# Performance work log

Hardware: AMD Instinct MI355X
Metric: run time of the kernel (lower is better)

## Reference

```python
import jax, jax.numpy as jnp
import numpy as np

D = 192          # embed_dim
DI = 2 * D       # d_inner (Mamba expand=2)
R = 12           # dt_rank = ceil(D / d_state)
N = 16           # d_state
DEPTH = 24
P = 16           # patch size
B = 4
SS, TS = 256, 128
PT = (TS // P) ** 2   # 64 template patches
PS = (SS // P) ** 2   # 256 search patches
L = PT + PS + 1       # 321 tokens (middle cls)


def setup_inputs() -> dict:
    key = jax.random.key(0)
    ks = jax.random.split(key, 24)
    f = lambda k, shp, s=0.02: (jax.random.normal(k, shp) * s).astype(jnp.float32)
    Alog = jnp.log(jnp.arange(1, N + 1, dtype=jnp.float32))  # S4D-real init
    Alog = jnp.tile(Alog, (DEPTH, DI, 1))
    return {
        "x_search": f(ks[0], (B, 3, SS, SS), 1.0),
        "x_template": f(ks[1], (B, 3, TS, TS), 1.0),
        "patch_w": f(ks[2], (D, 3, P, P)),
        "patch_b": jnp.zeros((D,), jnp.float32),
        "cls_token": f(ks[3], (1, 1, D)),
        "pos_embed": f(ks[4], (1, L, D)),
        "Win": f(ks[5], (DEPTH, 2 * DI, D)),
        "convw": f(ks[6], (DEPTH, DI, 4), 0.2),
        "convb": jnp.zeros((DEPTH, DI), jnp.float32),
        "Wx": f(ks[7], (DEPTH, R + 2 * N, DI)),
        "Wdt": f(ks[8], (DEPTH, DI, R), 0.1),
        "bdt": f(ks[9], (DEPTH, DI), 0.1),
        "Alog": Alog,
        "Dp": jnp.ones((DEPTH, DI), jnp.float32),
        "convw_b": f(ks[10], (DEPTH, DI, 4), 0.2),
        "convb_b": jnp.zeros((DEPTH, DI), jnp.float32),
        "Wx_b": f(ks[11], (DEPTH, R + 2 * N, DI)),
        "Wdt_b": f(ks[12], (DEPTH, DI, R), 0.1),
        "bdt_b": f(ks[13], (DEPTH, DI), 0.1),
        "Alog_b": Alog,
        "Dp_b": jnp.ones((DEPTH, DI), jnp.float32),
        "Wout": f(ks[14], (DEPTH, D, DI)),
        "normw": jnp.ones((DEPTH, D), jnp.float32),
        "normw_f": jnp.ones((D,), jnp.float32),
    }


def silu(x):
    return x * jax.nn.sigmoid(x)


def rmsnorm(x, w, eps=1e-5):
    return x * jax.lax.rsqrt(jnp.mean(x * x, -1, keepdims=True) + eps) * w


def patch_embed(x, w, b):
    # non-overlapping patch conv == blocked reshape + einsum
    Bn, C, H, W = x.shape
    xp = x.reshape(Bn, C, H // P, P, W // P, P)
    t = jnp.einsum('bcipjq,dcpq->bijd', xp, w)
    return t.reshape(Bn, (H // P) * (W // P), -1) + b


def causal_conv(u, w, b):
    # depthwise causal conv, kernel 4: u [B,DI,L], w [DI,4]
    Lx = u.shape[-1]
    up = jnp.pad(u, ((0, 0), (0, 0), (3, 0)))
    y = sum(w[:, k][None, :, None] * up[:, :, k:k + Lx] for k in range(4))
    return y + b[None, :, None]


def selective_scan(u, delta, A, Bm, Cm, Dp):
    # u, delta: [B,DI,L]; A: [DI,N]; Bm, Cm: [B,N,L]
    dA = jnp.exp(jnp.einsum('bdl,dn->lbdn', delta, A))
    dBu = jnp.einsum('bdl,bnl->lbdn', delta * u, Bm)

    def step(h, inp):
        dAt, dBut, ct = inp
        h = dAt * h + dBut
        return h, jnp.einsum('bdn,bn->bd', h, ct)

    h0 = jnp.zeros((u.shape[0], DI, N), u.dtype)
    _, ys = jax.lax.scan(step, h0, (dA, dBu, Cm.transpose(2, 0, 1)))
    y = ys.transpose(1, 2, 0)  # [B,DI,L]
    return y + Dp[None, :, None] * u


def _branch(x, z, convw, convb, Wx, Wdt, bdt, Alog, Dp):
    xc = silu(causal_conv(x, convw, convb))
    xdbl = jnp.einsum('bdl,ed->ble', xc, Wx)
    dt, Bm, Cm = xdbl[..., :R], xdbl[..., R:R + N], xdbl[..., R + N:]
    delta = jax.nn.softplus(jnp.einsum('blr,dr->bdl', dt, Wdt) + bdt[None, :, None])
    y = selective_scan(xc, delta, -jnp.exp(Alog), Bm.transpose(0, 2, 1),
                       Cm.transpose(0, 2, 1), Dp)
    return y * silu(z)


def _mixer(h, p):
    xz = jnp.einsum('bld,ed->ble', h, p['Win'])
    x = xz[..., :DI].transpose(0, 2, 1)   # [B,DI,L]
    z = xz[..., DI:].transpose(0, 2, 1)
    y = _branch(x, z, p['convw'], p['convb'], p['Wx'], p['Wdt'], p['bdt'],
                p['Alog'], p['Dp'])
    yb = _branch(x[..., ::-1], z[..., ::-1], p['convw_b'], p['convb_b'], p['Wx_b'],
                 p['Wdt_b'], p['bdt_b'], p['Alog_b'], p['Dp_b'])
    out = (y + yb[..., ::-1]) * 0.5  # bimamba v2 with if_divide_out
    return jnp.einsum('bdl,od->blo', out, p['Wout'])


def reference(x_search, x_template, patch_w, patch_b, cls_token, pos_embed,
              Win, convw, convb, Wx, Wdt, bdt, Alog, Dp,
              convw_b, convb_b, Wx_b, Wdt_b, bdt_b, Alog_b, Dp_b,
              Wout, normw, normw_f):
    ts = patch_embed(x_template, patch_w, patch_b)   # [B,64,D]
    ss = patch_embed(x_search, patch_w, patch_b)     # [B,256,D]
    tok = jnp.concatenate([ts, ss], 1)               # [B,320,D]
    mid = tok.shape[1] // 2
    cls = jnp.broadcast_to(cls_token, (tok.shape[0], 1, D))
    tok = jnp.concatenate([tok[:, :mid], cls, tok[:, mid:]], 1) + pos_embed

    lp = {'Win': Win, 'convw': convw, 'convb': convb, 'Wx': Wx, 'Wdt': Wdt,
          'bdt': bdt, 'Alog': Alog, 'Dp': Dp, 'convw_b': convw_b,
          'convb_b': convb_b, 'Wx_b': Wx_b, 'Wdt_b': Wdt_b, 'bdt_b': bdt_b,
          'Alog_b': Alog_b, 'Dp_b': Dp_b, 'Wout': Wout, 'normw': normw}

    def layer_step(carry, p):
        hidden, residual = carry
        residual = hidden + residual           # add
        hn = rmsnorm(residual, p['normw'])     # norm (fused_add_norm semantics)
        hidden = _mixer(hn, p)                 # mamba mixer
        return (hidden, residual), None

    (hidden, residual), _ = jax.lax.scan(layer_step, (tok, jnp.zeros_like(tok)), lp)
    return rmsnorm(hidden + residual, normw_f)   # final add + norm, [B,321,D]
```

## Files before the change

kernel.cpp:

```cpp
#include <hip/hip_runtime.h>
#include <math.h>

#define B_ 4
#define L_ 321
#define D_ 192
#define DI_ 384
#define E_ 768
#define R_ 12
#define N_ 16
#define DEPTH_ 24
#define XD 44

#define NC_ 21
#define LC_ 16

typedef __attribute__((ext_vector_type(8))) short bf16x8;
typedef __attribute__((ext_vector_type(4))) float f32x4;
typedef unsigned short ushort_t;

__device__ __forceinline__ float silu_f(float x) { return x / (1.f + __expf(-x)); }

__device__ __forceinline__ ushort_t f2bf(float x) {
    union { float f; unsigned u; } v; v.f = x;
    return (ushort_t)((v.u + 0x7fffu + ((v.u >> 16) & 1u)) >> 16);
}
__device__ __forceinline__ float bf2f(ushort_t h) {
    union { unsigned u; float f; } v; v.u = ((unsigned)h) << 16; return v.f;
}

__global__ void cvt_bf16(const float* __restrict__ src, ushort_t* __restrict__ dst, int n) {
    for (int i = blockIdx.x * blockDim.x + threadIdx.x; i < n; i += gridDim.x * blockDim.x)
        dst[i] = f2bf(src[i]);
}

__global__ void im2col_kernel(const float* __restrict__ xs, const float* __restrict__ xt,
                              ushort_t* __restrict__ pm) {
    int p_all = blockIdx.x % 320;
    int b = blockIdx.x / 320;
    const float* src; int i, j, W;
    if (p_all < 64) { int p = p_all; i = p >> 3; j = p & 7; W = 128; src = xt + (size_t)b*3*128*128; }
    else            { int p = p_all - 64; i = p >> 4; j = p & 15; W = 256; src = xs + (size_t)b*3*256*256; }
    ushort_t* dst = pm + (size_t)blockIdx.x * 768;
    for (int m = threadIdx.x; m < 768; m += blockDim.x) {
        int c = m >> 8, rem = m & 255, pp = rem >> 4, qq = rem & 15;
        dst[m] = f2bf(src[(size_t)(c*W + i*16 + pp)*W + j*16 + qq]);
    }
}

__global__ void tok_scatter(const float* __restrict__ tokmat, const float* __restrict__ pb,
                            const float* __restrict__ cls, const float* __restrict__ pos,
                            float* __restrict__ hidden, float* __restrict__ residual) {
    int blk = blockIdx.x;
    int b = blk / L_, t = blk % L_;
    int d = threadIdx.x;
    size_t o = (size_t)(b*L_ + t)*D_ + d;
    residual[o] = 0.f;
    float v;
    if (t == 160) v = cls[d];
    else {
        int p = (t < 160) ? t : t - 1;
        v = tokmat[(size_t)(b*320 + p)*D_ + d] + pb[d];
    }
    hidden[o] = v + pos[t*D_ + d];
}

template<int WM, int WN, int MFR, int NFR, int CMODE>
__global__ __launch_bounds__(WM*WN*64) void mfma_gemm(const ushort_t* __restrict__ A,
                          const ushort_t* __restrict__ Bw,
                          float* __restrict__ Cf, ushort_t* __restrict__ Ch,
                          int M, int N, int K) {
    constexpr int BM = WM * MFR * 16;
    constexpr int BN = WN * NFR * 16;
    int bx = blockIdx.x, by = blockIdx.y;
    int wave = threadIdx.x >> 6, lane = threadIdx.x & 63;
    int wr = wave / WN, wc = wave % WN;
    int m0 = by * BM + wr * MFR * 16;
    int n0 = bx * BN + wc * NFR * 16;
    int lrow = lane & 15;
    int lk   = (lane >> 4) * 8;

    f32x4 acc[MFR][NFR];
#pragma unroll
    for (int i = 0; i < MFR; ++i)
#pragma unroll
        for (int j = 0; j < NFR; ++j) acc[i][j] = (f32x4){0.f, 0.f, 0.f, 0.f};

    for (int k0 = 0; k0 < K; k0 += 32) {
        bf16x8 a[MFR], b[NFR];
#pragma unroll
        for (int i = 0; i < MFR; ++i) {
            int r = m0 + i*16 + lrow; r = min(r, M - 1);
            a[i] = *(const bf16x8*)(A + (size_t)r*K + k0 + lk);
        }
#pragma unroll
        for (int jn = 0; jn < NFR; ++jn) {
            int c = n0 + jn*16 + lrow; c = min(c, N - 1);
            b[jn] = *(const bf16x8*)(Bw + (size_t)c*K + k0 + lk);
        }
#pragma unroll
        for (int i = 0; i < MFR; ++i)
#pragma unroll
            for (int jn = 0; jn < NFR; ++jn)
                acc[i][jn] = __builtin_amdgcn_mfma_f32_16x16x32_bf16(a[i], b[jn], acc[i][jn], 0, 0, 0);
    }

    int crow = (lane >> 4) * 4;
    int ccol = lane & 15;
#pragma unroll
    for (int i = 0; i < MFR; ++i)
#pragma unroll
        for (int jn = 0; jn < NFR; ++jn) {
            int c = n0 + jn*16 + ccol;
            if (c >= N) continue;
#pragma unroll
            for (int j = 0; j < 4; ++j) {
                int r = m0 + i*16 + crow + j;
                if (r < M) {
                    if (CMODE == 0) Cf[(size_t)r*N + c] = acc[i][jn][j];
                    else            Ch[(size_t)r*N + c] = f2bf(acc[i][jn][j]);
                }
            }
        }
}

__global__ __launch_bounds__(64) void xdbl_dual(
    const ushort_t* __restrict__ xcf, const ushort_t* __restrict__ xcb,
    const ushort_t* __restrict__ Wxf, const ushort_t* __restrict__ Wxbw,
    float* __restrict__ xdf, float* __restrict__ xdb) {
    const int M = B_ * L_;
    int rev = blockIdx.y;
    const ushort_t* A  = rev ? xcb : xcf;
    const ushort_t* Bw = rev ? Wxbw : Wxf;
    float* C = rev ? xdb : xdf;
    int lane = threadIdx.x;
    int m0 = blockIdx.x * 16;
    int lrow = lane & 15, lk = (lane >> 4) * 8;

    f32x4 acc[3];
#pragma unroll
    for (int jn = 0; jn < 3; ++jn) acc[jn] = (f32x4){0.f, 0.f, 0.f, 0.f};

    for (int k0 = 0; k0 < DI_; k0 += 32) {
        int r = min(m0 + lrow, M - 1);
        bf16x8 a = *(const bf16x8*)(A + (size_t)r*DI_ + k0 + lk);
        bf16x8 b[3];
#pragma unroll
        for (int jn = 0; jn < 3; ++jn) {
            int c = min(jn*16 + lrow, XD - 1);
            b[jn] = *(const bf16x8*)(Bw + (size_t)c*DI_ + k0 + lk);
        }
#pragma unroll
        for (int jn = 0; jn < 3; ++jn)
            acc[jn] = __builtin_amdgcn_mfma_f32_16x16x32_bf16(a, b[jn], acc[jn], 0, 0, 0);
    }
    int crow = (lane >> 4) * 4, ccol = lane & 15;
#pragma unroll
    for (int jn = 0; jn < 3; ++jn) {
        int c = jn*16 + ccol;
        if (c >= XD) continue;
#pragma unroll
        for (int j = 0; j < 4; ++j) {
            int r = m0 + crow + j;
            if (r < M) C[(size_t)r*XD + c] = acc[jn][j];
        }
    }
}

__global__ __launch_bounds__(64) void outproj_gemm(
    const float* __restrict__ yf, const float* __restrict__ yb,
    const ushort_t* __restrict__ Ww, float* __restrict__ hidden) {
    const int M = B_*L_, Nn = D_, K = DI_;
    int lane = threadIdx.x;
    int m0 = blockIdx.y * 32;
    int n0 = blockIdx.x * 48;
    int lrow = lane & 15, lk = (lane >> 4) * 8;

    f32x4 acc[2][3];
#pragma unroll
    for (int i = 0; i < 2; ++i)
#pragma unroll
        for (int jn = 0; jn < 3; ++jn) acc[i][jn] = (f32x4){0.f, 0.f, 0.f, 0.f};

    for (int k0 = 0; k0 < K; k0 += 32) {
        bf16x8 a[2];
#pragma unroll
        for (int i = 0; i < 2; ++i) {
            int r = min(m0 + i*16 + lrow, M - 1);
            const float* p0 = yf + (size_t)r*K + k0 + lk;
            const float* p1 = yb + (size_t)r*K + k0 + lk;
            bf16x8 t;
#pragma unroll
            for (int j = 0; j < 8; ++j) t[j] = (short)f2bf(0.5f*(p0[j] + p1[j]));
            a[i] = t;
        }
        bf16x8 b[3];
#pragma unroll
        for (int jn = 0; jn < 3; ++jn) {
            int c = n0 + jn*16 + lrow;
            b[jn] = *(const bf16x8*)(Ww + (size_t)c*K + k0 + lk);
        }
#pragma unroll
        for (int i = 0; i < 2; ++i)
#pragma unroll
            for (int jn = 0; jn < 3; ++jn)
                acc[i][jn] = __builtin_amdgcn_mfma_f32_16x16x32_bf16(a[i], b[jn], acc[i][jn], 0, 0, 0);
    }
    int crow = (lane >> 4) * 4, ccol = lane & 15;
#pragma unroll
    for (int i = 0; i < 2; ++i)
#pragma unroll
        for (int jn = 0; jn < 3; ++jn) {
            int c = n0 + jn*16 + ccol;
#pragma unroll
            for (int j = 0; j < 4; ++j) {
                int r = m0 + i*16 + crow + j;
                if (r < M) hidden[(size_t)r*Nn + c] = acc[i][jn][j];
            }
        }
}

__global__ void prenorm_kernel(float* __restrict__ residual, const float* __restrict__ hidden,
                               const float* __restrict__ normw, ushort_t* __restrict__ hn) {
    int row = blockIdx.x;
    int tid = threadIdx.x;
    __shared__ float red[256];
    float v = 0.f;
    if (tid < D_) {
        v = residual[(size_t)row*D_ + tid] + hidden[(size_t)row*D_ + tid];
        residual[(size_t)row*D_ + tid] = v;
    }
    red[tid] = v * v;
    __syncthreads();
    for (int s = 128; s > 0; s >>= 1) { if (tid < s) red[tid] += red[tid + s]; __syncthreads(); }
    float scale = rsqrtf(red[0] / (float)D_ + 1e-5f);
    if (tid < D_) hn[(size_t)row*D_ + tid] = f2bf(v * scale * normw[tid]);
}

__global__ void final_kernel(const float* __restrict__ residual, const float* __restrict__ hidden,
                             const float* __restrict__ normw_f, float* __restrict__ out) {
    int row = blockIdx.x;
    int tid = threadIdx.x;
    __shared__ float red[256];
    float v = 0.f;
    if (tid < D_) v = residual[(size_t)row*D_ + tid] + hidden[(size_t)row*D_ + tid];
    red[tid] = v * v;
    __syncthreads();
    for (int s = 128; s > 0; s >>= 1) { if (tid < s) red[tid] += red[tid + s]; __syncthreads(); }
    float scale = rsqrtf(red[0] / (float)D_ + 1e-5f);
    if (tid < D_) out[(size_t)row*D_ + tid] = v * scale * normw_f[tid];
}

__global__ void conv_kernel(const ushort_t* __restrict__ xz,
                            const float* __restrict__ cw, const float* __restrict__ cb,
                            const float* __restrict__ cwb, const float* __restrict__ cbb,
                            ushort_t* __restrict__ xc_f, ushort_t* __restrict__ xc_b) {
    int blk = blockIdx.x;
    int b = blk / L_, l = blk % L_;
    int d = threadIdx.x;
    const ushort_t* xbase = xz + (size_t)b*L_*E_ + d;
    float acc = cb[d];
#pragma unroll
    for (int k = 0; k < 4; ++k) {
        int t = l - 3 + k;
        if (t >= 0) acc = fmaf(cw[d*4 + k], bf2f(xbase[(size_t)t*E_]), acc);
    }
    xc_f[(size_t)(b*L_ + l)*DI_ + d] = f2bf(silu_f(acc));
    float accb = cbb[d];
#pragma unroll
    for (int k = 0; k < 4; ++k) {
        int t = l - 3 + k;
        if (t >= 0) accb = fmaf(cwb[d*4 + k], bf2f(xbase[(size_t)(L_ - 1 - t)*E_]), accb);
    }
    xc_b[(size_t)(b*L_ + l)*DI_ + d] = f2bf(silu_f(accb));
}

__global__ __launch_bounds__(192) void scan_part1(
                           const ushort_t* __restrict__ xc_f, const ushort_t* __restrict__ xc_b,
                           const float* __restrict__ xdbl_f, const float* __restrict__ xdbl_b,
                           const float* __restrict__ Wdt, const float* __restrict__ bdt,
                           const float* __restrict__ Wdtb, const float* __restrict__ bdtb,
                           const float* __restrict__ Alog, const float* __restrict__ Alogb,
                           float* __restrict__ hloc, float* __restrict__ aprod) {
    int c = blockIdx.x, b = blockIdx.y >> 1, half = blockIdx.y & 1, br = blockIdx.z;
    int tid = threadIdx.x;
    int d = half * 192 + tid;
    const ushort_t* xc = br ? xc_b : xc_f;
    const float* xd = br ? xdbl_b : xdbl_f;
    const float* Wd = br ? Wdtb : Wdt;
    const float* bd = br ? bdtb : bdt;
    const float* Al = br ? Alogb : Alog;
    __shared__ float su[LC_][192];
    __shared__ float sdt[LC_][R_];
    __shared__ float sB[LC_][N_];
    int lbeg = c * LC_;
    int lend = min(lbeg + LC_, L_);
    int len = lend - lbeg;
    for (int l2 = 0; l2 < len; ++l2) {
        size_t row = (size_t)b*L_ + lbeg + l2;
        su[l2][tid] = bf2f(xc[row*DI_ + d]);
    }
    for (int idx = tid; idx < len*N_; idx += 192) {
        int l2 = idx >> 4, n = idx & 15;
        sB[l2][n] = xd[((size_t)b*L_ + lbeg + l2)*XD + R_ + n];
    }
    for (int idx = tid; idx < len*R_; idx += 192) {
        int l2 = idx / R_, r = idx % R_;
        sdt[l2][r] = xd[((size_t)b*L_ + lbeg + l2)*XD + r];
    }
    __syncthreads();
    float wreg[R_];
#pragma unroll
    for (int r = 0; r < R_; ++r) wreg[r] = Wd[d*R_ + r];
    float bdv = bd[d];
    float a[N_];
#pragma unroll
    for (int n = 0; n < N_; ++n) a[n] = -__expf(Al[d*N_ + n]);
    float h[N_], ap[N_];
#pragma unroll
    for (int n = 0; n < N_; ++n) { h[n] = 0.f; ap[n] = 1.f; }

    auto step = [&](int l2) {
        float dacc = bdv;
#pragma unroll
        for (int r = 0; r < R_; ++r) dacc = fmaf(wreg[r], sdt[l2][r], dacc);
        float dv = fmaxf(dacc, 0.f) + log1pf(__expf(-fabsf(dacc)));
        float u = su[l2][tid], du = dv * u;
#pragma unroll
        for (int n = 0; n < N_; ++n) {
            float e = __expf(dv * a[n]);
            h[n] = fmaf(e, h[n], du * sB[l2][n]);
            ap[n] *= e;
        }
    };
    if (len == LC_) {
#pragma unroll 4
        for (int l2 = 0; l2 < LC_; ++l2) step(l2);
    } else {
        for (int l2 = 0; l2 < len; ++l2) step(l2);
    }
    size_t base = (((size_t)(b*2 + br)*NC_ + c)*N_)*DI_ + d;
#pragma unroll
    for (int n = 0; n < N_; ++n) {
        hloc[base + (size_t)n*DI_]  = h[n];
        aprod[base + (size_t)n*DI_] = ap[n];
    }
}

__global__ void scan_combine(const float* __restrict__ hloc, const float* __restrict__ aprod,
                             float* __restrict__ hin) {
    int g = blockIdx.x * blockDim.x + threadIdx.x;
    int bb = g / (N_ * DI_);
    int rem = g % (N_ * DI_);
    float hrun = 0.f;
    for (int c = 0; c < NC_; ++c) {
        size_t idx = ((size_t)bb*NC_ + c)*N_*DI_ + rem;
        hin[idx] = hrun;
        hrun = fmaf(aprod[idx], hrun, hloc[idx]);
    }
}

__global__ __launch_bounds__(192) void scan_part3(
                           const ushort_t* __restrict__ xc_f, const ushort_t* __restrict__ xc_b,
                           const float* __restrict__ xdbl_f, const float* __restrict__ xdbl_b,
                           const float* __restrict__ Wdt, const float* __restrict__ bdt,
                           const float* __restrict__ Wdtb, const float* __restrict__ bdtb,
                           const ushort_t* __restrict__ xz,
                           const float* __restrict__ Alog, const float* __restrict__ Alogb,
                           const float* __restrict__ Dpf, const float* __restrict__ Dpb,
                           const float* __restrict__ hin,
                           float* __restrict__ y_f, float* __restrict__ y_b) {
    int c = blockIdx.x, b = blockIdx.y >> 1, half = blockIdx.y & 1, br = blockIdx.z;
    int tid = threadIdx.x;
    int d = half * 192 + tid;
    const ushort_t* xc = br ? xc_b : xc_f;
    const float* xd = br ? xdbl_b : xdbl_f;
    const float* Wd = br ? Wdtb : Wdt;
    const float* bd = br ? bdtb : bdt;
    const float* Al = br ? Alogb : Alog;
    const float* Dpp = br ? Dpb : Dpf;
    float* y = br ? y_b : y_f;
    __shared__ float su[LC_][192];
    __shared__ float sdt[LC_][R_];
    __shared__ float sB[LC_][N_];
    __shared__ float sC[LC_][N_];
    int lbeg = c * LC_;
    int lend = min(lbeg + LC_, L_);
    int len = lend - lbeg;
    for (int l2 = 0; l2 < len; ++l2) {
        size_t row = (size_t)b*L_ + lbeg + l2;
        su[l2][tid] = bf2f(xc[row*DI_ + d]);
    }
    for (int idx = tid; idx < len*N_; idx += 192) {
        int l2 = idx >> 4, n = idx & 15;
        size_t row = (size_t)b*L_ + lbeg + l2;
        sB[l2][n] = xd[row*XD + R_ + n];
        sC[l2][n] = xd[row*XD + R_ + N_ + n];
    }
    for (int idx = tid; idx < len*R_; idx += 192) {
        int l2 = idx / R_, r = idx % R_;
        sdt[l2][r] = xd[((size_t)b*L_ + lbeg + l2)*XD + r];
    }
    __syncthreads();
    float wreg[R_];
#pragma unroll
    for (int r = 0; r < R_; ++r) wreg[r] = Wd[d*R_ + r];
    float bdv = bd[d];
    float a[N_];
#pragma unroll
    for (int n = 0; n < N_; ++n) a[n] = -__expf(Al[d*N_ + n]);
    float h[N_];
    size_t hbase = (((size_t)(b*2 + br)*NC_ + c)*N_)*DI_ + d;
#pragma unroll
    for (int n = 0; n < N_; ++n) h[n] = hin[hbase + (size_t)n*DI_];
    float dpv = Dpp[d];

    auto step = [&](int l2) {
        float dacc = bdv;
#pragma unroll
        for (int r = 0; r < R_; ++r) dacc = fmaf(wreg[r], sdt[l2][r], dacc);
        float dv = fmaxf(dacc, 0.f) + log1pf(__expf(-fabsf(dacc)));
        float u = su[l2][tid], du = dv * u;
        float yv = 0.f;
#pragma unroll
        for (int n = 0; n < N_; ++n) {
            float e = __expf(dv * a[n]);
            h[n] = fmaf(e, h[n], du * sB[l2][n]);
            yv = fmaf(h[n], sC[l2][n], yv);
        }
        yv = fmaf(dpv, u, yv);
        int lo = br ? (L_ - 1 - (lbeg + l2)) : (lbeg + l2);
        float zv = bf2f(xz[((size_t)b*L_ + lo)*E_ + DI_ + d]);
        y[((size_t)b*L_ + lo)*DI_ + d] = yv * silu_f(zv);
    };
    if (len == LC_) {
#pragma unroll 4
        for (int l2 = 0; l2 < LC_; ++l2) step(l2);
    } else {
        for (int l2 = 0; l2 < len; ++l2) step(l2);
    }
}

extern "C" void kernel_launch(void* const* d_in, const int* in_sizes, int n_in,
                              void* d_out, int out_size, void* d_ws, size_t ws_size,
                              hipStream_t stream) {
    const float* xs     = (const float*)d_in[0];
    const float* xt     = (const float*)d_in[1];
    const float* pw     = (const float*)d_in[2];
    const float* pb     = (const float*)d_in[3];
    const float* cls    = (const float*)d_in[4];
    const float* pos    = (const float*)d_in[5];
    const float* Win    = (const float*)d_in[6];
    const float* convw  = (const float*)d_in[7];
    const float* convb  = (const float*)d_in[8];
    const float* Wx     = (const float*)d_in[9];
    const float* Wdt    = (const float*)d_in[10];
    const float* bdt    = (const float*)d_in[11];
    const float* Alog   = (const float*)d_in[12];
    const float* Dp     = (const float*)d_in[13];
    const float* convwb = (const float*)d_in[14];
    const float* convbb = (const float*)d_in[15];
    const float* Wxb    = (const float*)d_in[16];
    const float* Wdtb   = (const float*)d_in[17];
    const float* bdtb   = (const float*)d_in[18];
    const float* Alogb  = (const float*)d_in[19];
    const float* Dpb    = (const float*)d_in[20];
    const float* Wout   = (const float*)d_in[21];
    const float* normw  = (const float*)d_in[22];
    const float* normwf = (const float*)d_in[23];
    float* out = (float*)d_out;

    float* ws = (float*)d_ws;
    size_t off = 0;
    auto alloc = [&](size_t nfloats) { float* p = ws + off; off += nfloats; return p; };
    const size_t BL = (size_t)B_ * L_;
    const size_t CHNK = (size_t)B_ * 2 * NC_ * N_ * DI_;

    float*    residual = alloc(BL * D_);
    float*    hidden   = alloc(BL * D_);
    ushort_t* hn_bf    = (ushort_t*)alloc(BL * D_ / 2);
    ushort_t* xzb_bf   = (ushort_t*)alloc(BL * E_ / 2);
    ushort_t* xcf_bf   = (ushort_t*)alloc(BL * DI_ / 2);
    ushort_t* xcb_bf   = (ushort_t*)alloc(BL * DI_ / 2);
    float*    xdbl_f   = alloc(BL * XD);
    float*    xdbl_b   = alloc(BL * XD);
    float*    y_f      = alloc(BL * DI_);
    float*    y_b      = alloc(BL * DI_);
    float*    hloc     = alloc(CHNK);
    float*    aprod    = alloc(CHNK);
    float*    hin      = alloc(CHNK);
    ushort_t* pw_bf    = (ushort_t*)alloc((size_t)D_ * 768 / 2);
    ushort_t* Win_bf   = (ushort_t*)alloc((size_t)DEPTH_ * E_ * D_ / 2);
    ushort_t* Wx_bf    = (ushort_t*)alloc((size_t)DEPTH_ * XD * DI_ / 2);
    ushort_t* Wxb_bf   = (ushort_t*)alloc((size_t)DEPTH_ * XD * DI_ / 2);
    ushort_t* Wout_bf  = (ushort_t*)alloc((size_t)DEPTH_ * D_ * DI_ / 2);
    (void)ws_size; (void)in_sizes; (void)n_in; (void)out_size;

    cvt_bf16<<<dim3(64),   dim3(256), 0, stream>>>(pw,   pw_bf,   D_ * 768);
    cvt_bf16<<<dim3(2048), dim3(256), 0, stream>>>(Win,  Win_bf,  DEPTH_ * E_ * D_);
    cvt_bf16<<<dim3(512),  dim3(256), 0, stream>>>(Wx,   Wx_bf,   DEPTH_ * XD * DI_);
    cvt_bf16<<<dim3(512),  dim3(256), 0, stream>>>(Wxb,  Wxb_bf,  DEPTH_ * XD * DI_);
    cvt_bf16<<<dim3(1024), dim3(256), 0, stream>>>(Wout, Wout_bf, DEPTH_ * D_ * DI_);

    ushort_t* pmat   = (ushort_t*)y_f;
    float*    tokmat = y_b;
    im2col_kernel<<<dim3(B_ * 320), dim3(256), 0, stream>>>(xs, xt, pmat);
    mfma_gemm<2, 2, 2, 2, 0><<<dim3(3, 20), dim3(256), 0, stream>>>(
        pmat, pw_bf, tokmat, nullptr, B_ * 320, D_, 768);
    tok_scatter<<<dim3(B_ * L_), dim3(192), 0, stream>>>(tokmat, pb, cls, pos, hidden, residual);

    for (int layer = 0; layer < DEPTH_; ++layer) {
        const ushort_t* Win_l  = Win_bf  + (size_t)layer * E_ * D_;
        const ushort_t* Wx_l   = Wx_bf   + (size_t)layer * XD * DI_;
        const ushort_t* Wxb_l  = Wxb_bf  + (size_t)layer * XD * DI_;
        const ushort_t* Wout_l = Wout_bf + (size_t)layer * D_ * DI_;
        const float* cw_l    = convw  + (size_t)layer * DI_ * 4;
        const float* cb_l    = convb  + (size_t)layer * DI_;
        const float* cwb_l   = convwb + (size_t)layer * DI_ * 4;
        const float* cbb_l   = convbb + (size_t)layer * DI_;
        const float* Wdt_l   = Wdt    + (size_t)layer * DI_ * R_;
        const float* Wdtb_l  = Wdtb   + (size_t)layer * DI_ * R_;
        const float* bdt_l   = bdt    + (size_t)layer * DI_;
        const float* bdtb_l  = bdtb   + (size_t)layer * DI_;
        const float* Alog_l  = Alog   + (size_t)layer * DI_ * N_;
        const float* Alogb_l = Alogb  + (size_t)layer * DI_ * N_;
        const float* Dp_l    = Dp     + (size_t)layer * DI_;
        const float* Dpb_l   = Dpb    + (size_t)layer * DI_;
        const float* normw_l = normw  + (size_t)layer * D_;

        prenorm_kernel<<<dim3((int)BL), dim3(256), 0, stream>>>(residual, hidden, normw_l, hn_bf);
        mfma_gemm<2, 2, 2, 2, 1><<<dim3(12, 21), dim3(256), 0, stream>>>(
            hn_bf, Win_l, nullptr, xzb_bf, (int)BL, E_, D_);
        conv_kernel<<<dim3((int)BL), dim3(DI_), 0, stream>>>(
            xzb_bf, cw_l, cb_l, cwb_l, cbb_l, xcf_bf, xcb_bf);
        xdbl_dual<<<dim3(81, 2), dim3(64), 0, stream>>>(
            xcf_bf, xcb_bf, Wx_l, Wxb_l, xdbl_f, xdbl_b);
        scan_part1<<<dim3(NC_, B_ * 2, 2), dim3(192), 0, stream>>>(
            xcf_bf, xcb_bf, xdbl_f, xdbl_b, Wdt_l, bdt_l, Wdtb_l, bdtb_l,
            Alog_l, Alogb_l, hloc, aprod);
        scan_combine<<<dim3((B_*2*N_*DI_)/256), dim3(256), 0, stream>>>(hloc, aprod, hin);
        scan_part3<<<dim3(NC_, B_ * 2, 2), dim3(192), 0, stream>>>(
            xcf_bf, xcb_bf, xdbl_f, xdbl_b, Wdt_l, bdt_l, Wdtb_l, bdtb_l, xzb_bf,
            Alog_l, Alogb_l, Dp_l, Dpb_l, hin, y_f, y_b);
        outproj_gemm<<<dim3(4, 41), dim3(64), 0, stream>>>(y_f, y_b, Wout_l, hidden);
    }

    final_kernel<<<dim3((int)BL), dim3(256), 0, stream>>>(residual, hidden, normwf, out);
}
```

Measured before the change: 1.941 ms.

## Fuse in-projection with causal conv and out-projection with residual-add RMSNorm

Merges the in-projection GEMM with the depthwise causal conv (forward and reversed), so the x-half stays in shared memory and only z is written. The out-projection now adds the residual and applies the next layer's RMSNorm in its epilogue, which removes the separate prenorm and final kernels and the hidden buffer. The scan kernels read u straight into registers instead of staging it in shared memory. This cuts launches and global round-trips, at the cost of recomputing three halo rows per tile and running the out-projection as a 16-row grid with a cross-wave reduction.

```diff
diff --git a/kernel.cpp b/kernel.cpp
--- a/kernel.cpp
+++ b/kernel.cpp
@@ -49,25 +49,35 @@
 
 __global__ void tok_scatter(const float* __restrict__ tokmat, const float* __restrict__ pb,
                             const float* __restrict__ cls, const float* __restrict__ pos,
-                            float* __restrict__ hidden, float* __restrict__ residual) {
+                            float* __restrict__ residual) {
     int blk = blockIdx.x;
     int b = blk / L_, t = blk % L_;
     int d = threadIdx.x;
-    size_t o = (size_t)(b*L_ + t)*D_ + d;
-    residual[o] = 0.f;
     float v;
     if (t == 160) v = cls[d];
     else {
         int p = (t < 160) ? t : t - 1;
         v = tokmat[(size_t)(b*320 + p)*D_ + d] + pb[d];
     }
-    hidden[o] = v + pos[t*D_ + d];
-}
-
-template<int WM, int WN, int MFR, int NFR, int CMODE>
+    residual[(size_t)(b*L_ + t)*D_ + d] = v + pos[t*D_ + d];
+}
+
+__global__ void rms0_kernel(const float* __restrict__ residual, const float* __restrict__ normw,
+                            ushort_t* __restrict__ hn) {
+    int row = blockIdx.x;
+    int tid = threadIdx.x;
+    __shared__ float red[256];
+    float v = (tid < D_) ? residual[(size_t)row*D_ + tid] : 0.f;
+    red[tid] = v * v;
+    __syncthreads();
+    for (int s = 128; s > 0; s >>= 1) { if (tid < s) red[tid] += red[tid + s]; __syncthreads(); }
+    float scale = rsqrtf(red[0] / (float)D_ + 1e-5f);
+    if (tid < D_) hn[(size_t)row*D_ + tid] = f2bf(v * scale * normw[tid]);
+}
+
+template<int WM, int WN, int MFR, int NFR>
 __global__ __launch_bounds__(WM*WN*64) void mfma_gemm(const ushort_t* __restrict__ A,
-                          const ushort_t* __restrict__ Bw,
-                          float* __restrict__ Cf, ushort_t* __restrict__ Ch,
+                          const ushort_t* __restrict__ Bw, float* __restrict__ Cf,
                           int M, int N, int K) {
     constexpr int BM = WM * MFR * 16;
     constexpr int BN = WN * NFR * 16;
@@ -115,12 +125,86 @@
 #pragma unroll
             for (int j = 0; j < 4; ++j) {
                 int r = m0 + i*16 + crow + j;
-                if (r < M) {
-                    if (CMODE == 0) Cf[(size_t)r*N + c] = acc[i][jn][j];
-                    else            Ch[(size_t)r*N + c] = f2bf(acc[i][jn][j]);
-                }
+                if (r < M) Cf[(size_t)r*N + c] = acc[i][jn][j];
             }
         }
+}
+
+__global__ __launch_bounds__(256) void inproj_conv(
+    const ushort_t* __restrict__ hn, const ushort_t* __restrict__ Win_l,
+    const float* __restrict__ cw, const float* __restrict__ cb,
+    const float* __restrict__ cwb, const float* __restrict__ cbb,
+    ushort_t* __restrict__ xc_f, ushort_t* __restrict__ xc_b,
+    ushort_t* __restrict__ zbuf) {
+    int bx = blockIdx.x, by = blockIdx.y;
+    int b = by / 6, lm0 = (by % 6) * 64;
+    int wave = threadIdx.x >> 6, lane = threadIdx.x & 63;
+    int lrow = lane & 15, lk = (lane >> 4) * 8;
+    int ecol0 = bx * 64 + wave * 16;
+    bool xp = bx < 6;
+    int nf = xp ? 5 : 4;
+    int lbase = xp ? lm0 - 3 : lm0;
+
+    __shared__ float xt[80][68];
+
+    f32x4 acc[5];
+#pragma unroll
+    for (int fi = 0; fi < 5; ++fi) acc[fi] = (f32x4){0.f, 0.f, 0.f, 0.f};
+
+    for (int k0 = 0; k0 < D_; k0 += 32) {
+        bf16x8 bw = *(const bf16x8*)(Win_l + (size_t)(ecol0 + lrow)*D_ + k0 + lk);
+        for (int fi = 0; fi < nf; ++fi) {
+            int l = lbase + fi*16 + lrow;
+            l = min(max(l, 0), L_ - 1);
+            bf16x8 af = *(const bf16x8*)(hn + (size_t)(b*L_ + l)*D_ + k0 + lk);
+            acc[fi] = __builtin_amdgcn_mfma_f32_16x16x32_bf16(af, bw, acc[fi], 0, 0, 0);
+        }
+    }
+
+    int crow = (lane >> 4) * 4, ccol = lane & 15;
+    if (!xp) {
+#pragma unroll
+        for (int fi = 0; fi < 4; ++fi)
+#pragma unroll
+            for (int j = 0; j < 4; ++j) {
+                int l = lm0 + fi*16 + crow + j;
+                if (l < L_) zbuf[(size_t)(b*L_ + l)*DI_ + (ecol0 + ccol - DI_)] = f2bf(acc[fi][j]);
+            }
+        return;
+    }
+#pragma unroll
+    for (int fi = 0; fi < 5; ++fi)
+#pragma unroll
+        for (int j = 0; j < 4; ++j)
+            xt[fi*16 + crow + j][wave*16 + ccol] = acc[fi][j];
+    __syncthreads();
+
+    int dc = threadIdx.x & 63;
+    int lofs = threadIdx.x >> 6;
+    int d = bx*64 + dc;
+    float4 wf = *(const float4*)(cw + (size_t)d*4);
+    float4 wb = *(const float4*)(cwb + (size_t)d*4);
+    float bf0 = cb[d], bb0 = cbb[d];
+#pragma unroll
+    for (int i = 0; i < 16; ++i) {
+        int l2 = lofs + i*4;
+        int lf = lm0 + l2;
+        if (lf < L_) {
+            float a0 = bf0;
+#pragma unroll
+            for (int k = 0; k < 4; ++k)
+                if (lf - 3 + k >= 0) a0 = fmaf(((const float*)&wf)[k], xt[l2 + k][dc], a0);
+            xc_f[(size_t)(b*L_ + lf)*DI_ + d] = f2bf(silu_f(a0));
+        }
+        int lpp = (L_ - 1) - lm0 - l2;
+        if (lpp >= 0) {
+            float a1 = bb0;
+#pragma unroll
+            for (int k = 0; k < 4; ++k)
+                if (lpp - 3 + k >= 0) a1 = fmaf(((const float*)&wb)[k], xt[l2 + 6 - k][dc], a1);
+            xc_b[(size_t)(b*L_ + lpp)*DI_ + d] = f2bf(silu_f(a1));
+        }
+    }
 }
 
 __global__ __launch_bounds__(64) void xdbl_dual(
@@ -166,33 +250,29 @@
     }
 }
 
-__global__ __launch_bounds__(64) void outproj_gemm(
+template<bool LAST>
+__global__ __launch_bounds__(256) void outproj_fused(
     const float* __restrict__ yf, const float* __restrict__ yb,
-    const ushort_t* __restrict__ Ww, float* __restrict__ hidden) {
+    const ushort_t* __restrict__ Ww,
+    float* __restrict__ residual, const float* __restrict__ nw,
+    ushort_t* __restrict__ hn, float* __restrict__ outp) {
     const int M = B_*L_, Nn = D_, K = DI_;
-    int lane = threadIdx.x;
-    int m0 = blockIdx.y * 32;
-    int n0 = blockIdx.x * 48;
+    int wave = threadIdx.x >> 6, lane = threadIdx.x & 63;
+    int m0 = blockIdx.x * 16;
+    int n0 = wave * 48;
     int lrow = lane & 15, lk = (lane >> 4) * 8;
 
-    f32x4 acc[2][3];
-#pragma unroll
-    for (int i = 0; i < 2; ++i)
-#pragma unroll
-        for (int jn = 0; jn < 3; ++jn) acc[i][jn] = (f32x4){0.f, 0.f, 0.f, 0.f};
+    f32x4 acc[3];
+#pragma unroll
+    for (int jn = 0; jn < 3; ++jn) acc[jn] = (f32x4){0.f, 0.f, 0.f, 0.f};
 
     for (int k0 = 0; k0 < K; k0 += 32) {
-        bf16x8 a[2];
-#pragma unroll
-        for (int i = 0; i < 2; ++i) {
-            int r = min(m0 + i*16 + lrow, M - 1);
-            const float* p0 = yf + (size_t)r*K + k0 + lk;
-            const float* p1 = yb + (size_t)r*K + k0 + lk;
-            bf16x8 t;
-#pragma unroll
-            for (int j = 0; j < 8; ++j) t[j] = (short)f2bf(0.5f*(p0[j] + p1[j]));
-            a[i] = t;
-        }
+        int r = min(m0 + lrow, M - 1);
+        const float* p0 = yf + (size_t)r*K + k0 + lk;
+        const float* p1 = yb + (size_t)r*K + k0 + lk;
+        bf16x8 a;
+#pragma unroll
+        for (int j = 0; j < 8; ++j) a[j] = (short)f2bf(0.5f*(p0[j] + p1[j]));
         bf16x8 b[3];
 #pragma unroll
         for (int jn = 0; jn < 3; ++jn) {
@@ -200,78 +280,55 @@
             b[jn] = *(const bf16x8*)(Ww + (size_t)c*K + k0 + lk);
         }
 #pragma unroll
-        for (int i = 0; i < 2; ++i)
-#pragma unroll
-            for (int jn = 0; jn < 3; ++jn)
-                acc[i][jn] = __builtin_amdgcn_mfma_f32_16x16x32_bf16(a[i], b[jn], acc[i][jn], 0, 0, 0);
-    }
+        for (int jn = 0; jn < 3; ++jn)
+            acc[jn] = __builtin_amdgcn_mfma_f32_16x16x32_bf16(a, b[jn], acc[jn], 0, 0, 0);
+    }
+
     int crow = (lane >> 4) * 4, ccol = lane & 15;
-#pragma unroll
-    for (int i = 0; i < 2; ++i)
+    float resv[4][3];
+    float sq[4] = {0.f, 0.f, 0.f, 0.f};
+#pragma unroll
+    for (int j = 0; j < 4; ++j) {
+        int r = m0 + crow + j;
+        bool ok = r < M;
 #pragma unroll
         for (int jn = 0; jn < 3; ++jn) {
             int c = n0 + jn*16 + ccol;
-#pragma unroll
-            for (int j = 0; j < 4; ++j) {
-                int r = m0 + i*16 + crow + j;
-                if (r < M) hidden[(size_t)r*Nn + c] = acc[i][jn][j];
+            float v = ok ? (residual[(size_t)r*Nn + c] + acc[jn][j]) : 0.f;
+            resv[j][jn] = v;
+            sq[j] = fmaf(v, v, sq[j]);
+        }
+    }
+#pragma unroll
+    for (int m = 1; m < 16; m <<= 1)
+#pragma unroll
+        for (int j = 0; j < 4; ++j) sq[j] += __shfl_xor(sq[j], m, 64);
+
+    __shared__ float part[16][4];
+    if (ccol == 0) {
+#pragma unroll
+        for (int j = 0; j < 4; ++j) part[crow + j][wave] = sq[j];
+    }
+    __syncthreads();
+#pragma unroll
+    for (int j = 0; j < 4; ++j) {
+        int r = m0 + crow + j;
+        if (r >= M) continue;
+        int rt = crow + j;
+        float tot = part[rt][0] + part[rt][1] + part[rt][2] + part[rt][3];
+        float scale = rsqrtf(tot / (float)Nn + 1e-5f);
+#pragma unroll
+        for (int jn = 0; jn < 3; ++jn) {
+            int c = n0 + jn*16 + ccol;
+            float v = resv[j][jn];
+            if (LAST) {
+                outp[(size_t)r*Nn + c] = v * scale * nw[c];
+            } else {
+                residual[(size_t)r*Nn + c] = v;
+                hn[(size_t)r*Nn + c] = f2bf(v * scale * nw[c]);
             }
         }
-}
-
-__global__ void prenorm_kernel(float* __restrict__ residual, const float* __restrict__ hidden,
-                               const float* __restrict__ normw, ushort_t* __restrict__ hn) {
-    int row = blockIdx.x;
-    int tid = threadIdx.x;
-    __shared__ float red[256];
-    float v = 0.f;
-    if (tid < D_) {
-        v = residual[(size_t)row*D_ + tid] + hidden[(size_t)row*D_ + tid];
-        residual[(size_t)row*D_ + tid] = v;
-    }
-    red[tid] = v * v;
-    __syncthreads();
-    for (int s = 128; s > 0; s >>= 1) { if (tid < s) red[tid] += red[tid + s]; __syncthreads(); }
-    float scale = rsqrtf(red[0] / (float)D_ + 1e-5f);
-    if (tid < D_) hn[(size_t)row*D_ + tid] = f2bf(v * scale * normw[tid]);
-}
-
-__global__ void final_kernel(const float* __restrict__ residual, const float* __restrict__ hidden,
-                             const float* __restrict__ normw_f, float* __restrict__ out) {
-    int row = blockIdx.x;
-    int tid = threadIdx.x;
-    __shared__ float red[256];
-    float v = 0.f;
-    if (tid < D_) v = residual[(size_t)row*D_ + tid] + hidden[(size_t)row*D_ + tid];
-    red[tid] = v * v;
-    __syncthreads();
-    for (int s = 128; s > 0; s >>= 1) { if (tid < s) red[tid] += red[tid + s]; __syncthreads(); }
-    float scale = rsqrtf(red[0] / (float)D_ + 1e-5f);
-    if (tid < D_) out[(size_t)row*D_ + tid] = v * scale * normw_f[tid];
-}
-
-__global__ void conv_kernel(const ushort_t* __restrict__ xz,
-                            const float* __restrict__ cw, const float* __restrict__ cb,
-                            const float* __restrict__ cwb, const float* __restrict__ cbb,
-                            ushort_t* __restrict__ xc_f, ushort_t* __restrict__ xc_b) {
-    int blk = blockIdx.x;
-    int b = blk / L_, l = blk % L_;
-    int d = threadIdx.x;
-    const ushort_t* xbase = xz + (size_t)b*L_*E_ + d;
-    float acc = cb[d];
-#pragma unroll
-    for (int k = 0; k < 4; ++k) {
-        int t = l - 3 + k;
-        if (t >= 0) acc = fmaf(cw[d*4 + k], bf2f(xbase[(size_t)t*E_]), acc);
-    }
-    xc_f[(size_t)(b*L_ + l)*DI_ + d] = f2bf(silu_f(acc));
-    float accb = cbb[d];
-#pragma unroll
-    for (int k = 0; k < 4; ++k) {
-        int t = l - 3 + k;
-        if (t >= 0) accb = fmaf(cwb[d*4 + k], bf2f(xbase[(size_t)(L_ - 1 - t)*E_]), accb);
-    }
-    xc_b[(size_t)(b*L_ + l)*DI_ + d] = f2bf(silu_f(accb));
+    }
 }
 
 __global__ __launch_bounds__(192) void scan_part1(
@@ -289,16 +346,10 @@
     const float* Wd = br ? Wdtb : Wdt;
     const float* bd = br ? bdtb : bdt;
     const float* Al = br ? Alogb : Alog;
-    __shared__ float su[LC_][192];
     __shared__ float sdt[LC_][R_];
     __shared__ float sB[LC_][N_];
     int lbeg = c * LC_;
-    int lend = min(lbeg + LC_, L_);
-    int len = lend - lbeg;
-    for (int l2 = 0; l2 < len; ++l2) {
-        size_t row = (size_t)b*L_ + lbeg + l2;
-        su[l2][tid] = bf2f(xc[row*DI_ + d]);
-    }
+    int len = min(lbeg + LC_, L_) - lbeg;
     for (int idx = tid; idx < len*N_; idx += 192) {
         int l2 = idx >> 4, n = idx & 15;
         sB[l2][n] = xd[((size_t)b*L_ + lbeg + l2)*XD + R_ + n];
@@ -319,12 +370,12 @@
 #pragma unroll
     for (int n = 0; n < N_; ++n) { h[n] = 0.f; ap[n] = 1.f; }
 
-    auto step = [&](int l2) {
+    auto step = [&](int l2, float u) {
         float dacc = bdv;
 #pragma unroll
         for (int r = 0; r < R_; ++r) dacc = fmaf(wreg[r], sdt[l2][r], dacc);
         float dv = fmaxf(dacc, 0.f) + log1pf(__expf(-fabsf(dacc)));
-        float u = su[l2][tid], du = dv * u;
+        float du = dv * u;
 #pragma unroll
         for (int n = 0; n < N_; ++n) {
             float e = __expf(dv * a[n]);
@@ -333,10 +384,15 @@
         }
     };
     if (len == LC_) {
+        float u[LC_];
+#pragma unroll
+        for (int l2 = 0; l2 < LC_; ++l2)
+            u[l2] = bf2f(xc[((size_t)b*L_ + lbeg + l2)*DI_ + d]);
 #pragma unroll 4
-        for (int l2 = 0; l2 < LC_; ++l2) step(l2);
+        for (int l2 = 0; l2 < LC_; ++l2) step(l2, u[l2]);
     } else {
-        for (int l2 = 0; l2 < len; ++l2) step(l2);
+        for (int l2 = 0; l2 < len; ++l2)
+            step(l2, bf2f(xc[((size_t)b*L_ + lbeg + l2)*DI_ + d]));
     }
     size_t base = (((size_t)(b*2 + br)*NC_ + c)*N_)*DI_ + d;
 #pragma unroll
@@ -364,7 +420,7 @@
                            const float* __restrict__ xdbl_f, const float* __restrict__ xdbl_b,
                            const float* __restrict__ Wdt, const float* __restrict__ bdt,
                            const float* __restrict__ Wdtb, const float* __restrict__ bdtb,
-                           const ushort_t* __restrict__ xz,
+                           const ushort_t* __restrict__ zbuf,
                            const float* __restrict__ Alog, const float* __restrict__ Alogb,
                            const float* __restrict__ Dpf, const float* __restrict__ Dpb,
                            const float* __restrict__ hin,
@@ -379,17 +435,11 @@
     const float* Al = br ? Alogb : Alog;
     const float* Dpp = br ? Dpb : Dpf;
     float* y = br ? y_b : y_f;
-    __shared__ float su[LC_][192];
     __shared__ float sdt[LC_][R_];
     __shared__ float sB[LC_][N_];
     __shared__ float sC[LC_][N_];
     int lbeg = c * LC_;
-    int lend = min(lbeg + LC_, L_);
-    int len = lend - lbeg;
-    for (int l2 = 0; l2 < len; ++l2) {
-        size_t row = (size_t)b*L_ + lbeg + l2;
-        su[l2][tid] = bf2f(xc[row*DI_ + d]);
-    }
+    int len = min(lbeg + LC_, L_) - lbeg;
     for (int idx = tid; idx < len*N_; idx += 192) {
         int l2 = idx >> 4, n = idx & 15;
         size_t row = (size_t)b*L_ + lbeg + l2;
@@ -414,12 +464,12 @@
     for (int n = 0; n < N_; ++n) h[n] = hin[hbase + (size_t)n*DI_];
     float dpv = Dpp[d];
 
-    auto step = [&](int l2) {
+    auto step = [&](int l2, float u) {
         float dacc = bdv;
 #pragma unroll
         for (int r = 0; r < R_; ++r) dacc = fmaf(wreg[r], sdt[l2][r], dacc);
         float dv = fmaxf(dacc, 0.f) + log1pf(__expf(-fabsf(dacc)));
-        float u = su[l2][tid], du = dv * u;
+        float du = dv * u;
         float yv = 0.f;
 #pragma unroll
         for (int n = 0; n < N_; ++n) {
@@ -429,14 +479,19 @@
         }
         yv = fmaf(dpv, u, yv);
         int lo = br ? (L_ - 1 - (lbeg + l2)) : (lbeg + l2);
-        float zv = bf2f(xz[((size_t)b*L_ + lo)*E_ + DI_ + d]);
+        float zv = bf2f(zbuf[((size_t)b*L_ + lo)*DI_ + d]);
         y[((size_t)b*L_ + lo)*DI_ + d] = yv * silu_f(zv);
     };
     if (len == LC_) {
+        float u[LC_];
+#pragma unroll
+        for (int l2 = 0; l2 < LC_; ++l2)
+            u[l2] = bf2f(xc[((size_t)b*L_ + lbeg + l2)*DI_ + d]);
 #pragma unroll 4
-        for (int l2 = 0; l2 < LC_; ++l2) step(l2);
+        for (int l2 = 0; l2 < LC_; ++l2) step(l2, u[l2]);
     } else {
-        for (int l2 = 0; l2 < len; ++l2) step(l2);
+        for (int l2 = 0; l2 < len; ++l2)
+            step(l2, bf2f(xc[((size_t)b*L_ + lbeg + l2)*DI_ + d]));
     }
 }
 
@@ -476,9 +531,8 @@
     const size_t CHNK = (size_t)B_ * 2 * NC_ * N_ * DI_;
 
     float*    residual = alloc(BL * D_);
-    float*    hidden   = alloc(BL * D_);
     ushort_t* hn_bf    = (ushort_t*)alloc(BL * D_ / 2);
-    ushort_t* xzb_bf   = (ushort_t*)alloc(BL * E_ / 2);
+    ushort_t* zbuf     = (ushort_t*)alloc(BL * DI_ / 2);
     ushort_t* xcf_bf   = (ushort_t*)alloc(BL * DI_ / 2);
     ushort_t* xcb_bf   = (ushort_t*)alloc(BL * DI_ / 2);
     float*    xdbl_f   = alloc(BL * XD);
@@ -504,9 +558,10 @@
     ushort_t* pmat   = (ushort_t*)y_f;
     float*    tokmat = y_b;
     im2col_kernel<<<dim3(B_ * 320), dim3(256), 0, stream>>>(xs, xt, pmat);
-    mfma_gemm<2, 2, 2, 2, 0><<<dim3(3, 20), dim3(256), 0, stream>>>(
-        pmat, pw_bf, tokmat, nullptr, B_ * 320, D_, 768);
-    tok_scatter<<<dim3(B_ * L_), dim3(192), 0, stream>>>(tokmat, pb, cls, pos, hidden, residual);
+    mfma_gemm<2, 2, 2, 2><<<dim3(3, 20), dim3(256), 0, stream>>>(
+        pmat, pw_bf, tokmat, B_ * 320, D_, 768);
+    tok_scatter<<<dim3(B_ * L_), dim3(192), 0, stream>>>(tokmat, pb, cls, pos, residual);
+    rms0_kernel<<<dim3((int)BL), dim3(256), 0, stream>>>(residual, normw, hn_bf);
 
     for (int layer = 0; layer < DEPTH_; ++layer) {
         const ushort_t* Win_l  = Win_bf  + (size_t)layer * E_ * D_;
@@ -525,13 +580,9 @@
         const float* Alogb_l = Alogb  + (size_t)layer * DI_ * N_;
         const float* Dp_l    = Dp     + (size_t)layer * DI_;
         const float* Dpb_l   = Dpb    + (size_t)layer * DI_;
-        const float* normw_l = normw  + (size_t)layer * D_;
-
-        prenorm_kernel<<<dim3((int)BL), dim3(256), 0, stream>>>(residual, hidden, normw_l, hn_bf);
-        mfma_gemm<2, 2, 2, 2, 1><<<dim3(12, 21), dim3(256), 0, stream>>>(
-            hn_bf, Win_l, nullptr, xzb_bf, (int)BL, E_, D_);
-        conv_kernel<<<dim3((int)BL), dim3(DI_), 0, stream>>>(
-            xzb_bf, cw_l, cb_l, cwb_l, cbb_l, xcf_bf, xcb_bf);
+
+        inproj_conv<<<dim3(12, 24), dim3(256), 0, stream>>>(
+            hn_bf, Win_l, cw_l, cb_l, cwb_l, cbb_l, xcf_bf, xcb_bf, zbuf);
         xdbl_dual<<<dim3(81, 2), dim3(64), 0, stream>>>(
             xcf_bf, xcb_bf, Wx_l, Wxb_l, xdbl_f, xdbl_b);
         scan_part1<<<dim3(NC_, B_ * 2, 2), dim3(192), 0, stream>>>(
@@ -539,10 +590,14 @@
             Alog_l, Alogb_l, hloc, aprod);
         scan_combine<<<dim3((B_*2*N_*DI_)/256), dim3(256), 0, stream>>>(hloc, aprod, hin);
         scan_part3<<<dim3(NC_, B_ * 2, 2), dim3(192), 0, stream>>>(
-            xcf_bf, xcb_bf, xdbl_f, xdbl_b, Wdt_l, bdt_l, Wdtb_l, bdtb_l, xzb_bf,
+            xcf_bf, xcb_bf, xdbl_f, xdbl_b, Wdt_l, bdt_l, Wdtb_l, bdtb_l, zbuf,
             Alog_l, Alogb_l, Dp_l, Dpb_l, hin, y_f, y_b);
-        outproj_gemm<<<dim3(4, 41), dim3(64), 0, stream>>>(y_f, y_b, Wout_l, hidden);
-    }
-
-    final_kernel<<<dim3((int)BL), dim3(256), 0, stream>>>(residual, hidden, normwf, out);
-}
+        if (layer < DEPTH_ - 1) {
+            outproj_fused<false><<<dim3(81), dim3(256), 0, stream>>>(
+                y_f, y_b, Wout_l, residual, normw + (size_t)(layer + 1) * D_, hn_bf, nullptr);
+        } else {
+            outproj_fused<true><<<dim3(81), dim3(256), 0, stream>>>(
+                y_f, y_b, Wout_l, residual, normwf, nullptr, out);
+        }
+    }
+}
```

Result: slower. 2.040 ms (+5.1%).
